# Optimization experiments

Measured on AMD Instinct MI355X. Metric: run time of the kernel, lower is better.

## Reference

```python
import jax, jax.numpy as jnp
import numpy as np

N_NODES = 100000
N_EDGES = 1000000
C_IN, C_HID, C_OUT = 128, 64, 32


def _gcn_layer(x, W, b, src, dst, n):
    """PyG GCNConv with default add_self_loops=True, symmetric normalization.

    x: [N, in], W: [in, out], b: [out], src/dst: [E] int
    """
    h = x @ W  # [N, out] -- transform before aggregation
    # degree of each node counting the added self loop
    deg = jax.ops.segment_sum(jnp.ones_like(dst, dtype=h.dtype), dst, num_segments=n) + 1.0
    dinv = jax.lax.rsqrt(deg)  # deg >= 1 so always finite
    norm = dinv[src] * dinv[dst]  # [E]
    msg = h[src] * norm[:, None]  # [E, out]
    agg = jax.ops.segment_sum(msg, dst, num_segments=n)  # [N, out]
    # self-loop contribution: norm_ii = dinv_i * dinv_i
    out = agg + h * (dinv * dinv)[:, None]
    return out + b


def setup_inputs() -> dict:
    key = jax.random.key(0)
    k1, k2, k3, k4 = jax.random.split(key, 4)
    x = jax.random.normal(k1, (N_NODES, C_IN), dtype=jnp.float32)
    edge_index = jax.random.randint(k2, (2, N_EDGES), 0, N_NODES, dtype=jnp.int64)
    # Glorot-style init for the two GCN layers
    W1 = jax.random.normal(k3, (C_IN, C_HID), dtype=jnp.float32) / np.sqrt(C_IN)
    b1 = jnp.zeros((C_HID,), dtype=jnp.float32)
    W2 = jax.random.normal(k4, (C_HID, C_OUT), dtype=jnp.float32) / np.sqrt(C_HID)
    b2 = jnp.zeros((C_OUT,), dtype=jnp.float32)
    return {"x": x, "edge_index": edge_index, "W1": W1, "b1": b1, "W2": W2, "b2": b2}


def reference(x, edge_index, W1, b1, W2, b2):
    src, dst = edge_index[0], edge_index[1]
    n = x.shape[0]
    h = _gcn_layer(x, W1, b1, src, dst, n)
    h = jax.nn.relu(h)  # Dropout(0.1) is identity in eval mode
    out = _gcn_layer(h, W2, b2, src, dst, n)
    return out
```

## Files before the change

### kernel.cpp

```cpp
#include <hip/hip_runtime.h>

#define N_NODES 100000
#define N_EDGES 1000000
#define C_IN 128
#define C_HID 64
#define C_OUT 32
#define NB1 ((N_NODES + 255) / 256)
#define GT_BLOCKS ((N_NODES + 63) / 64)

__global__ __launch_bounds__(64) void k_detect(const unsigned int* __restrict__ ei,
                                               int* __restrict__ flag) {
    if (threadIdx.x == 0 && blockIdx.x == 0) {
        int is64 = 1;
        for (int i = 0; i < 64; ++i)
            if (ei[2 * i + 1] != 0u) { is64 = 0; break; }
        *flag = is64;
    }
}

__global__ __launch_bounds__(256) void k_rank(const unsigned int* __restrict__ ei,
                                              const int* __restrict__ flag,
                                              int* __restrict__ deg,
                                              int* __restrict__ rank) {
    const int T = gridDim.x * 256;
    const int t = blockIdx.x * 256 + threadIdx.x;
    const bool is64 = (*flag != 0);
    int d[4];
#pragma unroll
    for (int i = 0; i < 4; ++i) {
        int e = t + i * T;
        if (e < N_EDGES)
            d[i] = is64 ? ((const int2*)ei)[(size_t)N_EDGES + e].x
                        : (int)ei[(size_t)N_EDGES + e];
    }
    int r[4];
#pragma unroll
    for (int i = 0; i < 4; ++i) {
        int e = t + i * T;
        if (e < N_EDGES) r[i] = atomicAdd(&deg[d[i]], 1);
    }
#pragma unroll
    for (int i = 0; i < 4; ++i) {
        int e = t + i * T;
        if (e < N_EDGES) __builtin_nontemporal_store(r[i], &rank[e]);
    }
}

__global__ __launch_bounds__(256) void k_scan1(const int* __restrict__ deg,
                                               int* __restrict__ rowstart,
                                               int* __restrict__ blksum,
                                               float* __restrict__ dinv) {
    __shared__ int sm[256];
    int i = blockIdx.x * 256 + threadIdx.x;
    int v = (i < N_NODES) ? deg[i] : 0;
    if (i < N_NODES) dinv[i] = rsqrtf((float)v + 1.0f);
    sm[threadIdx.x] = v;
    __syncthreads();
    for (int o = 1; o < 256; o <<= 1) {
        int t = (threadIdx.x >= o) ? sm[threadIdx.x - o] : 0;
        __syncthreads();
        sm[threadIdx.x] += t;
        __syncthreads();
    }
    if (i < N_NODES) rowstart[i] = sm[threadIdx.x] - v;
    if (threadIdx.x == 255) blksum[blockIdx.x] = sm[255];
}

__global__ __launch_bounds__(512) void k_scan2(const int* __restrict__ blksum,
                                               int* __restrict__ blkoff) {
    __shared__ int sm[512];
    int v = (threadIdx.x < NB1) ? blksum[threadIdx.x] : 0;
    sm[threadIdx.x] = v;
    __syncthreads();
    for (int o = 1; o < 512; o <<= 1) {
        int t = (threadIdx.x >= o) ? sm[threadIdx.x - o] : 0;
        __syncthreads();
        sm[threadIdx.x] += t;
        __syncthreads();
    }
    if (threadIdx.x < NB1) blkoff[threadIdx.x] = sm[threadIdx.x] - v;
}

__global__ __launch_bounds__(256) void k_scan3(int* __restrict__ rowstart,
                                               const int* __restrict__ blkoff) {
    int i = blockIdx.x * 256 + threadIdx.x;
    if (i < N_NODES) rowstart[i] += blkoff[i >> 8];
    if (i == 0) rowstart[N_NODES] = N_EDGES;
}

__global__ __launch_bounds__(256) void k_fill2(const unsigned int* __restrict__ ei,
                                               const int* __restrict__ flag,
                                               const int* __restrict__ rowstart,
                                               const int* __restrict__ rank,
                                               int* __restrict__ esrc) {
    const int T = gridDim.x * 256;
    const int t = blockIdx.x * 256 + threadIdx.x;
    const bool is64 = (*flag != 0);
#pragma unroll
    for (int i = 0; i < 4; ++i) {
        int e = t + i * T;
        if (e < N_EDGES) {
            int s, d;
            if (is64) {
                s = ((const int2*)ei)[e].x;
                d = ((const int2*)ei)[(size_t)N_EDGES + e].x;
            } else {
                s = (int)ei[e];
                d = (int)ei[(size_t)N_EDGES + e];
            }
            int p = rowstart[d] + rank[e];
            __builtin_nontemporal_store(s, &esrc[p]);
        }
    }
}

__global__ __launch_bounds__(256) void k_gemm1(const float* __restrict__ x,
                                               const float* __restrict__ W1,
                                               const float* __restrict__ dinv,
                                               float* __restrict__ hs1) {
    __shared__ float w[C_IN * C_HID];
    __shared__ float xt[64 * C_IN];
    const int t = threadIdx.x;
    {
        const float4* W4 = (const float4*)W1;
        const float4* x4g = (const float4*)x;
        float4* w4 = (float4*)w;
        float4* xt4w = (float4*)xt;
        const size_t base = (size_t)blockIdx.x * 64 * (C_IN / 4);
        const size_t xmax = (size_t)N_NODES * (C_IN / 4) - 1;
#pragma unroll
        for (int j = 0; j < 8; ++j) {
            size_t idx = base + t + j * 256;
            if (idx > xmax) idx = xmax;
            xt4w[t + j * 256] = x4g[idx];
            w4[t + j * 256] = W4[t + j * 256];
        }
    }
    __syncthreads();
    const int c2 = t & 31;
    const int h  = (t >> 5) & 1;
    const int wid = t >> 6;
    const int lrow0 = wid * 16 + h * 8;
    const int grow0 = blockIdx.x * 64 + lrow0;
    const float4* xt4 = (const float4*)xt;

    float acc0[8] = {0, 0, 0, 0, 0, 0, 0, 0};
    float acc1[8] = {0, 0, 0, 0, 0, 0, 0, 0};
#pragma unroll 2
    for (int k4 = 0; k4 < C_IN / 4; ++k4) {
        float4 xv[8];
#pragma unroll
        for (int r = 0; r < 8; ++r)
            xv[r] = xt4[(lrow0 + r) * (C_IN / 4) + k4];
        float2 wv[4];
#pragma unroll
        for (int j = 0; j < 4; ++j)
            wv[j] = *reinterpret_cast<const float2*>(&w[(k4 * 4 + j) * C_HID + 2 * c2]);
#pragma unroll
        for (int r = 0; r < 8; ++r) {
            acc0[r] = fmaf(xv[r].x, wv[0].x, acc0[r]);
            acc1[r] = fmaf(xv[r].x, wv[0].y, acc1[r]);
            acc0[r] = fmaf(xv[r].y, wv[1].x, acc0[r]);
            acc1[r] = fmaf(xv[r].y, wv[1].y, acc1[r]);
            acc0[r] = fmaf(xv[r].z, wv[2].x, acc0[r]);
            acc1[r] = fmaf(xv[r].z, wv[2].y, acc1[r]);
            acc0[r] = fmaf(xv[r].w, wv[3].x, acc0[r]);
            acc1[r] = fmaf(xv[r].w, wv[3].y, acc1[r]);
        }
    }
#pragma unroll
    for (int r = 0; r < 8; ++r) {
        int rr = grow0 + r;
        if (rr < N_NODES) {
            float dv = dinv[rr];
            float2 o; o.x = acc0[r] * dv; o.y = acc1[r] * dv;
            *reinterpret_cast<float2*>(&hs1[(size_t)rr * C_HID + 2 * c2]) = o;
        }
    }
}

__global__ __launch_bounds__(256) void k_agg1(const int* __restrict__ rowstart,
                                              const int* __restrict__ esrc,
                                              const float* __restrict__ hs1,
                                              const float* __restrict__ dinv,
                                              const float* __restrict__ b1,
                                              float* __restrict__ y1) {
    int node = blockIdx.x * 4 + (threadIdx.x >> 6);
    int c = threadIdx.x & 63;
    int beg = rowstart[node], end = rowstart[node + 1];
    float acc = hs1[(size_t)node * C_HID + c];
    int j = beg;
    for (; j + 3 < end; j += 4) {
        int s0 = esrc[j], s1 = esrc[j + 1], s2 = esrc[j + 2], s3 = esrc[j + 3];
        float v0 = hs1[(size_t)s0 * C_HID + c];
        float v1 = hs1[(size_t)s1 * C_HID + c];
        float v2 = hs1[(size_t)s2 * C_HID + c];
        float v3 = hs1[(size_t)s3 * C_HID + c];
        acc += (v0 + v1) + (v2 + v3);
    }
    for (; j < end; ++j) acc += hs1[(size_t)esrc[j] * C_HID + c];
    y1[(size_t)node * C_HID + c] = fmaxf(fmaf(dinv[node], acc, b1[c]), 0.f);
}

__global__ __launch_bounds__(256) void k_gemm2(const float* __restrict__ y1,
                                               const float* __restrict__ W2,
                                               const float* __restrict__ dinv,
                                               float* __restrict__ hs2) {
    __shared__ float w[C_HID * C_OUT];
    __shared__ float yt[64 * C_HID];
    const int t = threadIdx.x;
    {
        const float4* W4 = (const float4*)W2;
        const float4* y4g = (const float4*)y1;
        float4* w4 = (float4*)w;
        float4* yt4w = (float4*)yt;
        const size_t base = (size_t)blockIdx.x * 64 * (C_HID / 4);
        const size_t ymax = (size_t)N_NODES * (C_HID / 4) - 1;
#pragma unroll
        for (int j = 0; j < 4; ++j) {
            size_t idx = base + t + j * 256;
            if (idx > ymax) idx = ymax;
            yt4w[t + j * 256] = y4g[idx];
        }
#pragma unroll
        for (int j = 0; j < 2; ++j)
            w4[t + j * 256] = W4[t + j * 256];
    }
    __syncthreads();
    const int c = t & 31;
    const int h = (t >> 5) & 1;
    const int wid = t >> 6;
    const int lrow0 = wid * 16 + h * 8;
    const int grow0 = blockIdx.x * 64 + lrow0;
    const float4* yt4 = (const float4*)yt;

    float acc[8] = {0, 0, 0, 0, 0, 0, 0, 0};
#pragma unroll 2
    for (int k4 = 0; k4 < C_HID / 4; ++k4) {
        float4 yv[8];
#pragma unroll
        for (int r = 0; r < 8; ++r)
            yv[r] = yt4[(lrow0 + r) * (C_HID / 4) + k4];
        float w0 = w[(k4 * 4 + 0) * C_OUT + c];
        float w1 = w[(k4 * 4 + 1) * C_OUT + c];
        float w2 = w[(k4 * 4 + 2) * C_OUT + c];
        float w3 = w[(k4 * 4 + 3) * C_OUT + c];
#pragma unroll
        for (int r = 0; r < 8; ++r) {
            acc[r] = fmaf(yv[r].x, w0, acc[r]);
            acc[r] = fmaf(yv[r].y, w1, acc[r]);
            acc[r] = fmaf(yv[r].z, w2, acc[r]);
            acc[r] = fmaf(yv[r].w, w3, acc[r]);
        }
    }
#pragma unroll
    for (int r = 0; r < 8; ++r) {
        int rr = grow0 + r;
        if (rr < N_NODES)
            hs2[(size_t)rr * C_OUT + c] = acc[r] * dinv[rr];
    }
}

__global__ __launch_bounds__(256) void k_agg2(const int* __restrict__ rowstart,
                                              const int* __restrict__ esrc,
                                              const float* __restrict__ hs2,
                                              const float* __restrict__ dinv,
                                              const float* __restrict__ b2,
                                              float* __restrict__ out) {
    int node = blockIdx.x * 8 + (threadIdx.x >> 5);
    int c = threadIdx.x & 31;
    int beg = rowstart[node], end = rowstart[node + 1];
    float acc = hs2[(size_t)node * C_OUT + c];
    int j = beg;
    for (; j + 3 < end; j += 4) {
        int s0 = esrc[j], s1 = esrc[j + 1], s2 = esrc[j + 2], s3 = esrc[j + 3];
        float v0 = hs2[(size_t)s0 * C_OUT + c];
        float v1 = hs2[(size_t)s1 * C_OUT + c];
        float v2 = hs2[(size_t)s2 * C_OUT + c];
        float v3 = hs2[(size_t)s3 * C_OUT + c];
        acc += (v0 + v1) + (v2 + v3);
    }
    for (; j < end; ++j) acc += hs2[(size_t)esrc[j] * C_OUT + c];
    out[(size_t)node * C_OUT + c] = fmaf(dinv[node], acc, b2[c]);
}

extern "C" void kernel_launch(void* const* d_in, const int* in_sizes, int n_in,
                              void* d_out, int out_size, void* d_ws, size_t ws_size,
                              hipStream_t stream) {
    const float* x  = (const float*)d_in[0];
    const unsigned int* ei = (const unsigned int*)d_in[1];
    const float* W1 = (const float*)d_in[2];
    const float* b1 = (const float*)d_in[3];
    const float* W2 = (const float*)d_in[4];
    const float* b2 = (const float*)d_in[5];
    float* out = (float*)d_out;

    char* ws = (char*)d_ws;
    size_t off = 0;
    auto take = [&](size_t bytes) {
        char* p = ws + off;
        off += (bytes + 255) & ~(size_t)255;
        return p;
    };
    int*   flag     = (int*)  take(256);
    int*   esrc     = (int*)  take((size_t)N_EDGES * 4);
    int*   rank     = (int*)  take((size_t)N_EDGES * 4);
    int*   deg      = (int*)  take((size_t)N_NODES * 4);
    int*   rowstart = (int*)  take((size_t)(N_NODES + 1) * 4);
    int*   blksum   = (int*)  take((size_t)NB1 * 4);
    int*   blkoff   = (int*)  take((size_t)NB1 * 4);
    float* dinv     = (float*)take((size_t)N_NODES * 4);
    float* hs1      = (float*)take((size_t)N_NODES * C_HID * 4);
    float* y1       = (float*)take((size_t)N_NODES * C_HID * 4);
    float* hs2      = (float*)take((size_t)N_NODES * C_OUT * 4);

    k_detect<<<1, 64, 0, stream>>>(ei, flag);
    hipMemsetAsync(deg, 0, (size_t)N_NODES * 4, stream);
    k_rank<<<1024, 256, 0, stream>>>(ei, flag, deg, rank);

    k_scan1<<<NB1, 256, 0, stream>>>(deg, rowstart, blksum, dinv);
    k_scan2<<<1, 512, 0, stream>>>(blksum, blkoff);
    k_scan3<<<NB1, 256, 0, stream>>>(rowstart, blkoff);

    k_fill2<<<1024, 256, 0, stream>>>(ei, flag, rowstart, rank, esrc);

    k_gemm1<<<GT_BLOCKS, 256, 0, stream>>>(x, W1, dinv, hs1);
    k_agg1<<<N_NODES / 4, 256, 0, stream>>>(rowstart, esrc, hs1, dinv, b1, y1);

    k_gemm2<<<GT_BLOCKS, 256, 0, stream>>>(y1, W2, dinv, hs2);
    k_agg2<<<N_NODES / 8, 256, 0, stream>>>(rowstart, esrc, hs2, dinv, b2, out);
}
```

Before: 311.1 us.

## Store transformed node features in fp16 and split edges across lanes in aggregation

The GEMM outputs (dinv-scaled transformed features) are now written as half2 instead of float, halving the bytes gathered per edge in both aggregation kernels. The aggregation kernels are restructured so each lane handles two channels via half2, and the spare lanes in a wave process interleaved edges, with partial sums combined by cross-lane shuffles. This is meant to cut gather bandwidth and memory transactions on the irregular neighbor reads. In exchange it introduces fp16 rounding of intermediate features, which may affect accuracy tolerance.

```diff
diff --git a/kernel.cpp b/kernel.cpp
--- a/kernel.cpp
+++ b/kernel.cpp
@@ -1,4 +1,5 @@
 #include <hip/hip_runtime.h>
+#include <hip/hip_fp16.h>
 
 #define N_NODES 100000
 #define N_EDGES 1000000
@@ -117,7 +118,7 @@
 __global__ __launch_bounds__(256) void k_gemm1(const float* __restrict__ x,
                                                const float* __restrict__ W1,
                                                const float* __restrict__ dinv,
-                                               float* __restrict__ hs1) {
+                                               __half* __restrict__ hs1h) {
     __shared__ float w[C_IN * C_HID];
     __shared__ float xt[64 * C_IN];
     const int t = threadIdx.x;
@@ -168,44 +169,60 @@
             acc1[r] = fmaf(xv[r].w, wv[3].y, acc1[r]);
         }
     }
+    __half2* h2o = (__half2*)hs1h;
 #pragma unroll
     for (int r = 0; r < 8; ++r) {
         int rr = grow0 + r;
         if (rr < N_NODES) {
             float dv = dinv[rr];
-            float2 o; o.x = acc0[r] * dv; o.y = acc1[r] * dv;
-            *reinterpret_cast<float2*>(&hs1[(size_t)rr * C_HID + 2 * c2]) = o;
+            h2o[(size_t)rr * 32 + c2] = __floats2half2_rn(acc0[r] * dv, acc1[r] * dv);
         }
     }
 }
 
 __global__ __launch_bounds__(256) void k_agg1(const int* __restrict__ rowstart,
                                               const int* __restrict__ esrc,
-                                              const float* __restrict__ hs1,
+                                              const __half* __restrict__ hs1h,
                                               const float* __restrict__ dinv,
                                               const float* __restrict__ b1,
                                               float* __restrict__ y1) {
-    int node = blockIdx.x * 4 + (threadIdx.x >> 6);
-    int c = threadIdx.x & 63;
-    int beg = rowstart[node], end = rowstart[node + 1];
-    float acc = hs1[(size_t)node * C_HID + c];
-    int j = beg;
-    for (; j + 3 < end; j += 4) {
-        int s0 = esrc[j], s1 = esrc[j + 1], s2 = esrc[j + 2], s3 = esrc[j + 3];
-        float v0 = hs1[(size_t)s0 * C_HID + c];
-        float v1 = hs1[(size_t)s1 * C_HID + c];
-        float v2 = hs1[(size_t)s2 * C_HID + c];
-        float v3 = hs1[(size_t)s3 * C_HID + c];
-        acc += (v0 + v1) + (v2 + v3);
-    }
-    for (; j < end; ++j) acc += hs1[(size_t)esrc[j] * C_HID + c];
-    y1[(size_t)node * C_HID + c] = fmaxf(fmaf(dinv[node], acc, b1[c]), 0.f);
+    const int node = blockIdx.x * 4 + (threadIdx.x >> 6);
+    const int lane = threadIdx.x & 63;
+    const int c2 = lane & 31;
+    const int eo = lane >> 5;
+    const __half2* h2 = (const __half2*)hs1h;
+    const int beg = rowstart[node], end = rowstart[node + 1];
+    float2 acc; acc.x = 0.f; acc.y = 0.f;
+    int j = beg + eo;
+    for (; j + 6 < end; j += 8) {
+        int s0 = esrc[j], s1 = esrc[j + 2], s2 = esrc[j + 4], s3 = esrc[j + 6];
+        float2 v0 = __half22float2(h2[(size_t)s0 * 32 + c2]);
+        float2 v1 = __half22float2(h2[(size_t)s1 * 32 + c2]);
+        float2 v2 = __half22float2(h2[(size_t)s2 * 32 + c2]);
+        float2 v3 = __half22float2(h2[(size_t)s3 * 32 + c2]);
+        acc.x += (v0.x + v1.x) + (v2.x + v3.x);
+        acc.y += (v0.y + v1.y) + (v2.y + v3.y);
+    }
+    for (; j < end; j += 2) {
+        float2 v = __half22float2(h2[(size_t)esrc[j] * 32 + c2]);
+        acc.x += v.x; acc.y += v.y;
+    }
+    acc.x += __shfl_xor(acc.x, 32);
+    acc.y += __shfl_xor(acc.y, 32);
+    if (eo == 0) {
+        float2 self = __half22float2(h2[(size_t)node * 32 + c2]);
+        float dv = dinv[node];
+        float2 o;
+        o.x = fmaxf(fmaf(dv, acc.x + self.x, b1[2 * c2]), 0.f);
+        o.y = fmaxf(fmaf(dv, acc.y + self.y, b1[2 * c2 + 1]), 0.f);
+        reinterpret_cast<float2*>(y1)[(size_t)node * 32 + c2] = o;
+    }
 }
 
 __global__ __launch_bounds__(256) void k_gemm2(const float* __restrict__ y1,
                                                const float* __restrict__ W2,
                                                const float* __restrict__ dinv,
-                                               float* __restrict__ hs2) {
+                                               __half* __restrict__ hs2h) {
     __shared__ float w[C_HID * C_OUT];
     __shared__ float yt[64 * C_HID];
     const int t = threadIdx.x;
@@ -227,61 +244,88 @@
             w4[t + j * 256] = W4[t + j * 256];
     }
     __syncthreads();
-    const int c = t & 31;
-    const int h = (t >> 5) & 1;
+    const int c2 = t & 15;
+    const int rg = (t >> 4) & 3;
     const int wid = t >> 6;
-    const int lrow0 = wid * 16 + h * 8;
+    const int lrow0 = wid * 16 + rg * 4;
     const int grow0 = blockIdx.x * 64 + lrow0;
     const float4* yt4 = (const float4*)yt;
 
-    float acc[8] = {0, 0, 0, 0, 0, 0, 0, 0};
+    float2 acc[4];
+#pragma unroll
+    for (int r = 0; r < 4; ++r) { acc[r].x = 0.f; acc[r].y = 0.f; }
 #pragma unroll 2
     for (int k4 = 0; k4 < C_HID / 4; ++k4) {
-        float4 yv[8];
-#pragma unroll
-        for (int r = 0; r < 8; ++r)
+        float4 yv[4];
+#pragma unroll
+        for (int r = 0; r < 4; ++r)
             yv[r] = yt4[(lrow0 + r) * (C_HID / 4) + k4];
-        float w0 = w[(k4 * 4 + 0) * C_OUT + c];
-        float w1 = w[(k4 * 4 + 1) * C_OUT + c];
-        float w2 = w[(k4 * 4 + 2) * C_OUT + c];
-        float w3 = w[(k4 * 4 + 3) * C_OUT + c];
-#pragma unroll
-        for (int r = 0; r < 8; ++r) {
-            acc[r] = fmaf(yv[r].x, w0, acc[r]);
-            acc[r] = fmaf(yv[r].y, w1, acc[r]);
-            acc[r] = fmaf(yv[r].z, w2, acc[r]);
-            acc[r] = fmaf(yv[r].w, w3, acc[r]);
-        }
-    }
-#pragma unroll
-    for (int r = 0; r < 8; ++r) {
+        float2 wv[4];
+#pragma unroll
+        for (int j = 0; j < 4; ++j)
+            wv[j] = *reinterpret_cast<const float2*>(&w[(k4 * 4 + j) * C_OUT + 2 * c2]);
+#pragma unroll
+        for (int r = 0; r < 4; ++r) {
+            acc[r].x = fmaf(yv[r].x, wv[0].x, acc[r].x);
+            acc[r].y = fmaf(yv[r].x, wv[0].y, acc[r].y);
+            acc[r].x = fmaf(yv[r].y, wv[1].x, acc[r].x);
+            acc[r].y = fmaf(yv[r].y, wv[1].y, acc[r].y);
+            acc[r].x = fmaf(yv[r].z, wv[2].x, acc[r].x);
+            acc[r].y = fmaf(yv[r].z, wv[2].y, acc[r].y);
+            acc[r].x = fmaf(yv[r].w, wv[3].x, acc[r].x);
+            acc[r].y = fmaf(yv[r].w, wv[3].y, acc[r].y);
+        }
+    }
+    __half2* h2o = (__half2*)hs2h;
+#pragma unroll
+    for (int r = 0; r < 4; ++r) {
         int rr = grow0 + r;
-        if (rr < N_NODES)
-            hs2[(size_t)rr * C_OUT + c] = acc[r] * dinv[rr];
+        if (rr < N_NODES) {
+            float dv = dinv[rr];
+            h2o[(size_t)rr * 16 + c2] = __floats2half2_rn(acc[r].x * dv, acc[r].y * dv);
+        }
     }
 }
 
 __global__ __launch_bounds__(256) void k_agg2(const int* __restrict__ rowstart,
                                               const int* __restrict__ esrc,
-                                              const float* __restrict__ hs2,
+                                              const __half* __restrict__ hs2h,
                                               const float* __restrict__ dinv,
                                               const float* __restrict__ b2,
                                               float* __restrict__ out) {
-    int node = blockIdx.x * 8 + (threadIdx.x >> 5);
-    int c = threadIdx.x & 31;
-    int beg = rowstart[node], end = rowstart[node + 1];
-    float acc = hs2[(size_t)node * C_OUT + c];
-    int j = beg;
-    for (; j + 3 < end; j += 4) {
-        int s0 = esrc[j], s1 = esrc[j + 1], s2 = esrc[j + 2], s3 = esrc[j + 3];
-        float v0 = hs2[(size_t)s0 * C_OUT + c];
-        float v1 = hs2[(size_t)s1 * C_OUT + c];
-        float v2 = hs2[(size_t)s2 * C_OUT + c];
-        float v3 = hs2[(size_t)s3 * C_OUT + c];
-        acc += (v0 + v1) + (v2 + v3);
-    }
-    for (; j < end; ++j) acc += hs2[(size_t)esrc[j] * C_OUT + c];
-    out[(size_t)node * C_OUT + c] = fmaf(dinv[node], acc, b2[c]);
+    const int node = blockIdx.x * 4 + (threadIdx.x >> 6);
+    const int lane = threadIdx.x & 63;
+    const int c2 = lane & 15;
+    const int eo = lane >> 4;
+    const __half2* h2 = (const __half2*)hs2h;
+    const int beg = rowstart[node], end = rowstart[node + 1];
+    float2 acc; acc.x = 0.f; acc.y = 0.f;
+    int j = beg + eo;
+    for (; j + 12 < end; j += 16) {
+        int s0 = esrc[j], s1 = esrc[j + 4], s2 = esrc[j + 8], s3 = esrc[j + 12];
+        float2 v0 = __half22float2(h2[(size_t)s0 * 16 + c2]);
+        float2 v1 = __half22float2(h2[(size_t)s1 * 16 + c2]);
+        float2 v2 = __half22float2(h2[(size_t)s2 * 16 + c2]);
+        float2 v3 = __half22float2(h2[(size_t)s3 * 16 + c2]);
+        acc.x += (v0.x + v1.x) + (v2.x + v3.x);
+        acc.y += (v0.y + v1.y) + (v2.y + v3.y);
+    }
+    for (; j < end; j += 4) {
+        float2 v = __half22float2(h2[(size_t)esrc[j] * 16 + c2]);
+        acc.x += v.x; acc.y += v.y;
+    }
+    acc.x += __shfl_xor(acc.x, 16);
+    acc.y += __shfl_xor(acc.y, 16);
+    acc.x += __shfl_xor(acc.x, 32);
+    acc.y += __shfl_xor(acc.y, 32);
+    if (eo == 0) {
+        float2 self = __half22float2(h2[(size_t)node * 16 + c2]);
+        float dv = dinv[node];
+        float2 o;
+        o.x = fmaf(dv, acc.x + self.x, b2[2 * c2]);
+        o.y = fmaf(dv, acc.y + self.y, b2[2 * c2 + 1]);
+        reinterpret_cast<float2*>(out)[(size_t)node * 16 + c2] = o;
+    }
 }
 
 extern "C" void kernel_launch(void* const* d_in, const int* in_sizes, int n_in,
@@ -302,17 +346,17 @@
         off += (bytes + 255) & ~(size_t)255;
         return p;
     };
-    int*   flag     = (int*)  take(256);
-    int*   esrc     = (int*)  take((size_t)N_EDGES * 4);
-    int*   rank     = (int*)  take((size_t)N_EDGES * 4);
-    int*   deg      = (int*)  take((size_t)N_NODES * 4);
-    int*   rowstart = (int*)  take((size_t)(N_NODES + 1) * 4);
-    int*   blksum   = (int*)  take((size_t)NB1 * 4);
-    int*   blkoff   = (int*)  take((size_t)NB1 * 4);
-    float* dinv     = (float*)take((size_t)N_NODES * 4);
-    float* hs1      = (float*)take((size_t)N_NODES * C_HID * 4);
-    float* y1       = (float*)take((size_t)N_NODES * C_HID * 4);
-    float* hs2      = (float*)take((size_t)N_NODES * C_OUT * 4);
+    int*    flag     = (int*)   take(256);
+    int*    esrc     = (int*)   take((size_t)N_EDGES * 4);
+    int*    rank     = (int*)   take((size_t)N_EDGES * 4);
+    int*    deg      = (int*)   take((size_t)N_NODES * 4);
+    int*    rowstart = (int*)   take((size_t)(N_NODES + 1) * 4);
+    int*    blksum   = (int*)   take((size_t)NB1 * 4);
+    int*    blkoff   = (int*)   take((size_t)NB1 * 4);
+    float*  dinv     = (float*) take((size_t)N_NODES * 4);
+    __half* hs1h     = (__half*)take((size_t)N_NODES * C_HID * 2);
+    float*  y1       = (float*) take((size_t)N_NODES * C_HID * 4);
+    __half* hs2h     = (__half*)take((size_t)N_NODES * C_OUT * 2);
 
     k_detect<<<1, 64, 0, stream>>>(ei, flag);
     hipMemsetAsync(deg, 0, (size_t)N_NODES * 4, stream);
@@ -324,9 +368,9 @@
 
     k_fill2<<<1024, 256, 0, stream>>>(ei, flag, rowstart, rank, esrc);
 
-    k_gemm1<<<GT_BLOCKS, 256, 0, stream>>>(x, W1, dinv, hs1);
-    k_agg1<<<N_NODES / 4, 256, 0, stream>>>(rowstart, esrc, hs1, dinv, b1, y1);
-
-    k_gemm2<<<GT_BLOCKS, 256, 0, stream>>>(y1, W2, dinv, hs2);
-    k_agg2<<<N_NODES / 8, 256, 0, stream>>>(rowstart, esrc, hs2, dinv, b2, out);
-}
+    k_gemm1<<<GT_BLOCKS, 256, 0, stream>>>(x, W1, dinv, hs1h);
+    k_agg1<<<N_NODES / 4, 256, 0, stream>>>(rowstart, esrc, hs1h, dinv, b1, y1);
+
+    k_gemm2<<<GT_BLOCKS, 256, 0, stream>>>(y1, W2, dinv, hs2h);
+    k_agg2<<<N_NODES / 4, 256, 0, stream>>>(rowstart, esrc, hs2h, dinv, b2, out);
+}
```

After: 310.7 us. No clear change (-0.1%).
